# Optimization experiments

Hardware: AMD Instinct MI355X
Metric: run time of the kernel (lower is better)

## Reference

```python
import jax, jax.numpy as jnp
import numpy as np

N, IN_DIM, LDIM = 8192, 512, 256
NEG_SLOPE = 0.01  # torch F.leaky_relu default
EPS = 1e-10


def setup_inputs() -> dict:
    key = jax.random.key(0)
    k1, k2, k3, k4 = jax.random.split(key, 4)
    x = jax.random.normal(k1, (N, IN_DIM), dtype=jnp.float32)
    adj = jax.random.uniform(k2, (N, N), dtype=jnp.float32)
    # nn.Linear(in_dim, learning_dim, bias=False) weight: [learning_dim, in_dim]
    proj_w = jax.random.normal(k3, (LDIM, IN_DIM), dtype=jnp.float32) * (1.0 / np.sqrt(IN_DIM))
    # nn.init.uniform_(learn_w, a=0, b=1)
    learn_w = jax.random.uniform(k4, (LDIM,), dtype=jnp.float32)
    return {"x": x, "adj": adj, "proj_w": proj_w, "learn_w": learn_w}


def reference(x, adj, proj_w, learn_w):
    # x_hat = projection(x): [N, LDIM]
    x_hat = x @ proj_w.T
    # cosine-distance score: sum_d w_d * (1 - xn_i[d] * xn_j[d])
    #   = sum(w) - (xn * w) @ xn.T  -- avoids the N x N x D intermediate
    xn = x_hat / jnp.linalg.norm(x_hat, axis=-1, keepdims=True)  # [N, LDIM]
    scores = jnp.sum(learn_w) - jnp.einsum('id,jd->ij', xn * learn_w, xn)  # [N, N]
    out = jax.nn.leaky_relu(scores, NEG_SLOPE)
    out = out - jnp.max(out, axis=-1, keepdims=True)
    soft_adj = adj * jnp.exp(out)
    soft_adj = soft_adj / jnp.sum(soft_adj, axis=-1, keepdims=True) + EPS
    return soft_adj
```

## Files before the change

### kernel.cpp

```cpp
#include <hip/hip_runtime.h>
#include <stdint.h>

#define NN 8192
#define KDIM 512
#define LDIM 256

typedef short bf16x8 __attribute__((ext_vector_type(8)));
typedef short short8 __attribute__((ext_vector_type(8)));
typedef float f32x4 __attribute__((ext_vector_type(4)));
typedef unsigned short u16x4 __attribute__((ext_vector_type(4)));

__device__ __forceinline__ unsigned short f2bf(float f) {
  unsigned int u = __float_as_uint(f);
  u = (u + 0x7fffu + ((u >> 16) & 1u)) >> 16;
  return (unsigned short)u;
}
__device__ __forceinline__ float bf2f(unsigned short s) {
  return __uint_as_float(((unsigned int)s) << 16);
}

__device__ __forceinline__ void async_ld16(const unsigned short* g, void* l) {
  __builtin_amdgcn_global_load_lds(
      (const __attribute__((address_space(1))) unsigned int*)g,
      (__attribute__((address_space(3))) unsigned int*)l, 16, 0, 0);
}

__global__ __launch_bounds__(256) void cast_kernel(
    const float* __restrict__ x, const float* __restrict__ pw,
    unsigned short* __restrict__ xb, unsigned short* __restrict__ pwb) {
  const int i = blockIdx.x * 256 + threadIdx.x;
  float4 v = ((const float4*)x)[i];
  u16x4 o;
  o[0] = (short)f2bf(v.x); o[1] = (short)f2bf(v.y);
  o[2] = (short)f2bf(v.z); o[3] = (short)f2bf(v.w);
  ((u16x4*)xb)[i] = o;
  if (i < (LDIM * KDIM) / 4) {
    float4 w = ((const float4*)pw)[i];
    u16x4 ow;
    ow[0] = (short)f2bf(w.x); ow[1] = (short)f2bf(w.y);
    ow[2] = (short)f2bf(w.z); ow[3] = (short)f2bf(w.w);
    ((u16x4*)pwb)[i] = ow;
  }
}

__global__ __launch_bounds__(256) void gemm1_norm_kernel(
    const unsigned short* __restrict__ xb,
    const unsigned short* __restrict__ pwb,
    const float* __restrict__ w,
    unsigned short* __restrict__ Ab, unsigned short* __restrict__ Bb) {
  __shared__ alignas(16) unsigned short As[32 * 32];
  __shared__ alignas(16) unsigned short Bs[256 * 32];
  __shared__ float nrm[32][5];
  __shared__ float wS[LDIM];
  __shared__ alignas(16) unsigned short xnS[32][264];
  __shared__ alignas(16) unsigned short anS[32][264];

  const int tid = threadIdx.x;
  const int wave = tid >> 6;
  const int lane = tid & 63;
  const int quad = lane >> 4;
  const int l16 = lane & 15;
  const size_t row0 = (size_t)blockIdx.x * 32;

  if (tid < LDIM) wS[tid] = w[tid];

  f32x4 acc[2][4];
#pragma unroll
  for (int i = 0; i < 2; ++i)
#pragma unroll
    for (int j = 0; j < 4; ++j) acc[i][j] = (f32x4)(0.0f);

  for (int k0 = 0; k0 < KDIM; k0 += 32) {
#pragma unroll
    for (int j = 0; j < 4; ++j) {
      const int c = (wave * 4 + j) * 64 + lane;
      async_ld16(pwb + (size_t)(c >> 2) * KDIM + (c & 3) * 8 + k0,
                 (char*)Bs + (wave * 4 + j) * 1024);
    }
    if (wave == 0) {
#pragma unroll
      for (int j2 = 0; j2 < 2; ++j2) {
        const int c = j2 * 64 + lane;
        async_ld16(xb + (row0 + (c >> 2)) * (size_t)KDIM + (c & 3) * 8 + k0,
                   (char*)As + j2 * 1024);
      }
    }
    __syncthreads();
    bf16x8 av[2], bv[4];
#pragma unroll
    for (int mt = 0; mt < 2; ++mt)
      av[mt] = *(const bf16x8*)(As + (mt * 16 + l16) * 32 + quad * 8);
#pragma unroll
    for (int nt = 0; nt < 4; ++nt)
      bv[nt] = *(const bf16x8*)(Bs + (wave * 64 + nt * 16 + l16) * 32 + quad * 8);
#pragma unroll
    for (int mt = 0; mt < 2; ++mt)
#pragma unroll
      for (int nt = 0; nt < 4; ++nt)
        acc[mt][nt] = __builtin_amdgcn_mfma_f32_16x16x32_bf16(
            av[mt], bv[nt], acc[mt][nt], 0, 0, 0);
    __syncthreads();
  }

#pragma unroll
  for (int mt = 0; mt < 2; ++mt)
#pragma unroll
    for (int r = 0; r < 4; ++r) {
      float s = 0.0f;
#pragma unroll
      for (int nt = 0; nt < 4; ++nt) s += acc[mt][nt][r] * acc[mt][nt][r];
      s += __shfl_xor(s, 1);
      s += __shfl_xor(s, 2);
      s += __shfl_xor(s, 4);
      s += __shfl_xor(s, 8);
      if (l16 == 0) nrm[mt * 16 + quad * 4 + r][wave] = s;
    }
  __syncthreads();
  if (tid < 32)
    nrm[tid][4] = rsqrtf(nrm[tid][0] + nrm[tid][1] + nrm[tid][2] + nrm[tid][3]);
  __syncthreads();

#pragma unroll
  for (int mt = 0; mt < 2; ++mt)
#pragma unroll
    for (int r = 0; r < 4; ++r) {
      const int row = mt * 16 + quad * 4 + r;
      const float inv = nrm[row][4];
#pragma unroll
      for (int nt = 0; nt < 4; ++nt) {
        const int col = wave * 64 + nt * 16 + l16;
        const float xn = acc[mt][nt][r] * inv;
        xnS[row][col] = f2bf(xn);
        anS[row][col] = f2bf(xn * wS[col]);
      }
    }
  __syncthreads();

  {
    const int row = tid >> 3;
    const int cb = (tid & 7) * 32;
    unsigned short* bdst = Bb + (row0 + row) * LDIM + cb;
    unsigned short* adst = Ab + (row0 + row) * LDIM + cb;
#pragma unroll
    for (int q = 0; q < 4; ++q) {
      ((short8*)bdst)[q] = *(const short8*)&xnS[row][cb + q * 8];
      ((short8*)adst)[q] = *(const short8*)&anS[row][cb + q * 8];
    }
  }
}

template <int K, int MODE>
__global__ __launch_bounds__(256) void gemm_bt(
    const unsigned short* __restrict__ A,
    const unsigned short* __restrict__ B,
    float* __restrict__ C,
    unsigned short* __restrict__ T,
    const float* __restrict__ adj,
    float* __restrict__ rowsum) {
  __shared__ unsigned short As[128 * 32];
  __shared__ unsigned short Bs[128 * 32];
  __shared__ float rs[128];
  __shared__ float trans[32 * 132];

  const int tid = threadIdx.x;
  const int wave = tid >> 6;
  const int lane = tid & 63;
  const int quad = lane >> 4;
  const int l16 = lane & 15;
  const int wm = wave >> 1;
  const int wn = wave & 1;

  const int lin = blockIdx.y * 64 + blockIdx.x;
  const int swz = (lin & 7) * 512 + (lin >> 3);
  const size_t row0 = (size_t)(swz >> 6) * 128;
  const size_t col0 = (size_t)(swz & 63) * 128;

  const int c0 = wave * 128 + lane;
  const int mA = c0 >> 2;
  const int kA = (c0 & 3) * 8;
  const unsigned short* Ag = A + (row0 + mA) * (size_t)K + kA;
  const unsigned short* Bg = B + (col0 + mA) * (size_t)K + kA;
  char* AsB = (char*)As;
  char* BsB = (char*)Bs;
  unsigned short* dA0 = (unsigned short*)(AsB + wave * 2048);
  unsigned short* dA1 = (unsigned short*)(AsB + wave * 2048 + 1024);
  unsigned short* dB0 = (unsigned short*)(BsB + wave * 2048);
  unsigned short* dB1 = (unsigned short*)(BsB + wave * 2048 + 1024);

  f32x4 acc[4][4];
#pragma unroll
  for (int i = 0; i < 4; ++i)
#pragma unroll
    for (int j = 0; j < 4; ++j) acc[i][j] = (f32x4)(0.0f);

  for (int k0 = 0; k0 < K; k0 += 32) {
    async_ld16(Ag + k0, dA0);
    async_ld16(Ag + 16 * (size_t)K + k0, dA1);
    async_ld16(Bg + k0, dB0);
    async_ld16(Bg + 16 * (size_t)K + k0, dB1);
    __syncthreads();

    bf16x8 av[4], bv[4];
#pragma unroll
    for (int mt = 0; mt < 4; ++mt)
      av[mt] = *(const bf16x8*)(AsB + (wm * 64 + mt * 16 + l16) * 64 + quad * 16);
#pragma unroll
    for (int nt = 0; nt < 4; ++nt)
      bv[nt] = *(const bf16x8*)(BsB + (wn * 64 + nt * 16 + l16) * 64 + quad * 16);
#pragma unroll
    for (int mt = 0; mt < 4; ++mt)
#pragma unroll
      for (int nt = 0; nt < 4; ++nt)
        acc[mt][nt] = __builtin_amdgcn_mfma_f32_16x16x32_bf16(av[mt], bv[nt], acc[mt][nt], 0, 0, 0);
    __syncthreads();
  }

  const int s = tid >> 3;
  const int cb = tid & 7;
  const int coff = cb * 16;
#pragma unroll
  for (int mt = 0; mt < 4; ++mt) {
    __syncthreads();
#pragma unroll
    for (int nt = 0; nt < 4; ++nt)
#pragma unroll
      for (int r = 0; r < 4; ++r)
        trans[(wm * 16 + quad * 4 + r) * 132 + wn * 64 + nt * 16 + l16] =
            acc[mt][nt][r];
    __syncthreads();
    const size_t gr = row0 + (size_t)(s >> 4) * 64 + mt * 16 + (s & 15);
    const float* arow = adj + gr * NN + col0 + coff;
    float av16[16];
#pragma unroll
    for (int q = 0; q < 4; ++q) {
      float4 a4 = ((const float4*)arow)[q];
      av16[q * 4 + 0] = a4.x;
      av16[q * 4 + 1] = a4.y;
      av16[q * 4 + 2] = a4.z;
      av16[q * 4 + 3] = a4.w;
    }
    const float* drow = &trans[s * 132 + coff];
    float part = 0.0f;
    if constexpr (MODE == 1) {
      short8 p0, p1;
#pragma unroll
      for (int j = 0; j < 16; ++j) {
        float tv = av16[j] * __expf(-drow[j]);
        unsigned short us = f2bf(tv);
        part += bf2f(us);
        if (j < 8) p0[j] = (short)us; else p1[j - 8] = (short)us;
      }
      short8* trow = (short8*)(T + gr * NN + col0 + coff);
      trow[0] = p0;
      trow[1] = p1;
    } else {
      float4 o[4];
#pragma unroll
      for (int j = 0; j < 16; ++j) {
        float tv = av16[j] * __expf(-drow[j]);
        part += tv;
        ((float*)o)[j] = tv;
      }
      float4* crow = (float4*)(C + gr * NN + col0 + coff);
#pragma unroll
      for (int q = 0; q < 4; ++q) crow[q] = o[q];
    }
    part += __shfl_xor(part, 1);
    part += __shfl_xor(part, 2);
    part += __shfl_xor(part, 4);
    if (cb == 0) rs[(s >> 4) * 64 + mt * 16 + (s & 15)] = part;
  }
  __syncthreads();
  if (tid < 128) atomicAdd(&rowsum[row0 + tid], rs[tid]);
}

__global__ __launch_bounds__(256) void scale_bf16_kernel(
    const unsigned short* __restrict__ T, const float* __restrict__ rowsum,
    float* __restrict__ out) {
  const size_t i = (size_t)blockIdx.x * 256 + threadIdx.x;
  const int row = (int)(i >> 10);
  short8 tv = ((const short8*)T)[i];
  const float inv = 1.0f / rowsum[row];
  float4 o0, o1;
  o0.x = bf2f((unsigned short)tv[0]) * inv + 1e-10f;
  o0.y = bf2f((unsigned short)tv[1]) * inv + 1e-10f;
  o0.z = bf2f((unsigned short)tv[2]) * inv + 1e-10f;
  o0.w = bf2f((unsigned short)tv[3]) * inv + 1e-10f;
  o1.x = bf2f((unsigned short)tv[4]) * inv + 1e-10f;
  o1.y = bf2f((unsigned short)tv[5]) * inv + 1e-10f;
  o1.z = bf2f((unsigned short)tv[6]) * inv + 1e-10f;
  o1.w = bf2f((unsigned short)tv[7]) * inv + 1e-10f;
  ((float4*)out)[i * 2] = o0;
  ((float4*)out)[i * 2 + 1] = o1;
}

__global__ __launch_bounds__(256) void scale_f32_kernel(
    float* __restrict__ t, const float* __restrict__ rowsum) {
  const size_t i = (size_t)blockIdx.x * 256 + threadIdx.x;
  const int row = (int)(i >> 11);
  float4 v = ((float4*)t)[i];
  const float inv = 1.0f / rowsum[row];
  v.x = v.x * inv + 1e-10f;
  v.y = v.y * inv + 1e-10f;
  v.z = v.z * inv + 1e-10f;
  v.w = v.w * inv + 1e-10f;
  ((float4*)t)[i] = v;
}

extern "C" void kernel_launch(void* const* d_in, const int* in_sizes, int n_in,
                              void* d_out, int out_size, void* d_ws, size_t ws_size,
                              hipStream_t stream) {
  (void)in_sizes; (void)n_in; (void)out_size;
  const float* x   = (const float*)d_in[0];
  const float* adj = (const float*)d_in[1];
  const float* pw  = (const float*)d_in[2];
  const float* lw  = (const float*)d_in[3];
  float* out = (float*)d_out;
  char* ws = (char*)d_ws;

  unsigned short* xb   = (unsigned short*)(ws);
  unsigned short* pwb  = (unsigned short*)(ws + 8388608);
  unsigned short* Ab   = (unsigned short*)(ws + 17039360);
  unsigned short* Bb   = (unsigned short*)(ws + 21233664);
  float*          rsum = (float*)(ws + 25427968);
  unsigned short* Tbuf = (unsigned short*)(ws + 25460736);
  const bool big_ws = ws_size >= 25460736ull + (size_t)NN * NN * 2ull;

  cast_kernel<<<(NN * KDIM) / (256 * 4), 256, 0, stream>>>(x, pw, xb, pwb);
  gemm1_norm_kernel<<<NN / 32, 256, 0, stream>>>(xb, pwb, lw, Ab, Bb);
  hipMemsetAsync(rsum, 0, NN * sizeof(float), stream);
  if (big_ws) {
    gemm_bt<LDIM, 1><<<dim3(64, 64), 256, 0, stream>>>(Ab, Bb, nullptr, Tbuf, adj, rsum);
    scale_bf16_kernel<<<(NN / 8) * (NN / 256), 256, 0, stream>>>(Tbuf, rsum, out);
  } else {
    gemm_bt<LDIM, 2><<<dim3(64, 64), 256, 0, stream>>>(Ab, Bb, out, nullptr, adj, rsum);
    scale_f32_kernel<<<(NN / 4) * (NN / 256), 256, 0, stream>>>(out, rsum);
  }
}
```

Baseline: 545.5 us.

## Fuse x bf16 cast into projection GEMM and shrink epilogue staging for occupancy

The x-to-bf16 cast moves into the projection GEMM kernel, which loads its 32-row fp32 tile directly into LDS, removing a separate pass that wrote and reread an 8 MB intermediate. The main fused GEMM/softmax kernel halves its epilogue transpose buffer by staging one 64-row half at a time, and adds a launch-bounds occupancy hint of 5 blocks. The cost is more barriers in the epilogue, narrower per-thread adj loads, and a larger LDS footprint in the first GEMM kernel.

```diff
diff --git a/kernel.cpp b/kernel.cpp
--- a/kernel.cpp
+++ b/kernel.cpp
@@ -25,30 +25,22 @@
       (__attribute__((address_space(3))) unsigned int*)l, 16, 0, 0);
 }
 
-__global__ __launch_bounds__(256) void cast_kernel(
-    const float* __restrict__ x, const float* __restrict__ pw,
-    unsigned short* __restrict__ xb, unsigned short* __restrict__ pwb) {
+__global__ __launch_bounds__(256) void cast_pw_kernel(
+    const float* __restrict__ pw, unsigned short* __restrict__ pwb) {
   const int i = blockIdx.x * 256 + threadIdx.x;
-  float4 v = ((const float4*)x)[i];
-  u16x4 o;
-  o[0] = (short)f2bf(v.x); o[1] = (short)f2bf(v.y);
-  o[2] = (short)f2bf(v.z); o[3] = (short)f2bf(v.w);
-  ((u16x4*)xb)[i] = o;
-  if (i < (LDIM * KDIM) / 4) {
-    float4 w = ((const float4*)pw)[i];
-    u16x4 ow;
-    ow[0] = (short)f2bf(w.x); ow[1] = (short)f2bf(w.y);
-    ow[2] = (short)f2bf(w.z); ow[3] = (short)f2bf(w.w);
-    ((u16x4*)pwb)[i] = ow;
-  }
+  float4 w = ((const float4*)pw)[i];
+  u16x4 ow;
+  ow[0] = (short)f2bf(w.x); ow[1] = (short)f2bf(w.y);
+  ow[2] = (short)f2bf(w.z); ow[3] = (short)f2bf(w.w);
+  ((u16x4*)pwb)[i] = ow;
 }
 
 __global__ __launch_bounds__(256) void gemm1_norm_kernel(
-    const unsigned short* __restrict__ xb,
+    const float* __restrict__ x,
     const unsigned short* __restrict__ pwb,
     const float* __restrict__ w,
     unsigned short* __restrict__ Ab, unsigned short* __restrict__ Bb) {
-  __shared__ alignas(16) unsigned short As[32 * 32];
+  __shared__ alignas(16) unsigned short Axl[32 * 520];
   __shared__ alignas(16) unsigned short Bs[256 * 32];
   __shared__ float nrm[32][5];
   __shared__ float wS[LDIM];
@@ -64,6 +56,21 @@
 
   if (tid < LDIM) wS[tid] = w[tid];
 
+  {
+    const float4* xr = (const float4*)(x + row0 * KDIM);
+#pragma unroll
+    for (int rnd = 0; rnd < 16; ++rnd) {
+      const int idx = rnd * 256 + tid;
+      float4 v = xr[idx];
+      u16x4 o;
+      o[0] = (short)f2bf(v.x); o[1] = (short)f2bf(v.y);
+      o[2] = (short)f2bf(v.z); o[3] = (short)f2bf(v.w);
+      const int e = idx * 4;
+      *(u16x4*)&Axl[(e >> 9) * 520 + (e & 511)] = o;
+    }
+  }
+  __syncthreads();
+
   f32x4 acc[2][4];
 #pragma unroll
   for (int i = 0; i < 2; ++i)
@@ -77,19 +84,11 @@
       async_ld16(pwb + (size_t)(c >> 2) * KDIM + (c & 3) * 8 + k0,
                  (char*)Bs + (wave * 4 + j) * 1024);
     }
-    if (wave == 0) {
-#pragma unroll
-      for (int j2 = 0; j2 < 2; ++j2) {
-        const int c = j2 * 64 + lane;
-        async_ld16(xb + (row0 + (c >> 2)) * (size_t)KDIM + (c & 3) * 8 + k0,
-                   (char*)As + j2 * 1024);
-      }
-    }
     __syncthreads();
     bf16x8 av[2], bv[4];
 #pragma unroll
     for (int mt = 0; mt < 2; ++mt)
-      av[mt] = *(const bf16x8*)(As + (mt * 16 + l16) * 32 + quad * 8);
+      av[mt] = *(const bf16x8*)(Axl + (mt * 16 + l16) * 520 + k0 + quad * 8);
 #pragma unroll
     for (int nt = 0; nt < 4; ++nt)
       bv[nt] = *(const bf16x8*)(Bs + (wave * 64 + nt * 16 + l16) * 32 + quad * 8);
@@ -150,7 +149,7 @@
 }
 
 template <int K, int MODE>
-__global__ __launch_bounds__(256) void gemm_bt(
+__global__ __launch_bounds__(256, 5) void gemm_bt(
     const unsigned short* __restrict__ A,
     const unsigned short* __restrict__ B,
     float* __restrict__ C,
@@ -160,7 +159,7 @@
   __shared__ unsigned short As[128 * 32];
   __shared__ unsigned short Bs[128 * 32];
   __shared__ float rs[128];
-  __shared__ float trans[32 * 132];
+  __shared__ float trans[16 * 132];
 
   const int tid = threadIdx.x;
   const int wave = tid >> 6;
@@ -215,60 +214,64 @@
     __syncthreads();
   }
 
-  const int s = tid >> 3;
-  const int cb = tid & 7;
-  const int coff = cb * 16;
+  const int sr = tid >> 4;
+  const int cb = tid & 15;
+  const int coff = cb * 8;
 #pragma unroll
   for (int mt = 0; mt < 4; ++mt) {
-    __syncthreads();
-#pragma unroll
-    for (int nt = 0; nt < 4; ++nt)
-#pragma unroll
-      for (int r = 0; r < 4; ++r)
-        trans[(wm * 16 + quad * 4 + r) * 132 + wn * 64 + nt * 16 + l16] =
-            acc[mt][nt][r];
-    __syncthreads();
-    const size_t gr = row0 + (size_t)(s >> 4) * 64 + mt * 16 + (s & 15);
-    const float* arow = adj + gr * NN + col0 + coff;
-    float av16[16];
-#pragma unroll
-    for (int q = 0; q < 4; ++q) {
-      float4 a4 = ((const float4*)arow)[q];
-      av16[q * 4 + 0] = a4.x;
-      av16[q * 4 + 1] = a4.y;
-      av16[q * 4 + 2] = a4.z;
-      av16[q * 4 + 3] = a4.w;
-    }
-    const float* drow = &trans[s * 132 + coff];
-    float part = 0.0f;
-    if constexpr (MODE == 1) {
-      short8 p0, p1;
-#pragma unroll
-      for (int j = 0; j < 16; ++j) {
-        float tv = av16[j] * __expf(-drow[j]);
-        unsigned short us = f2bf(tv);
-        part += bf2f(us);
-        if (j < 8) p0[j] = (short)us; else p1[j - 8] = (short)us;
+#pragma unroll
+    for (int wh = 0; wh < 2; ++wh) {
+      __syncthreads();
+      if (wm == wh) {
+#pragma unroll
+        for (int nt = 0; nt < 4; ++nt)
+#pragma unroll
+          for (int r = 0; r < 4; ++r)
+            trans[(quad * 4 + r) * 132 + wn * 64 + nt * 16 + l16] =
+                acc[mt][nt][r];
       }
-      short8* trow = (short8*)(T + gr * NN + col0 + coff);
-      trow[0] = p0;
-      trow[1] = p1;
-    } else {
-      float4 o[4];
-#pragma unroll
-      for (int j = 0; j < 16; ++j) {
-        float tv = av16[j] * __expf(-drow[j]);
-        part += tv;
-        ((float*)o)[j] = tv;
+      __syncthreads();
+      const size_t gr = row0 + (size_t)wh * 64 + mt * 16 + sr;
+      const float* arow = adj + gr * NN + col0 + coff;
+      float av8[8];
+#pragma unroll
+      for (int q = 0; q < 2; ++q) {
+        float4 a4 = ((const float4*)arow)[q];
+        av8[q * 4 + 0] = a4.x;
+        av8[q * 4 + 1] = a4.y;
+        av8[q * 4 + 2] = a4.z;
+        av8[q * 4 + 3] = a4.w;
       }
-      float4* crow = (float4*)(C + gr * NN + col0 + coff);
-#pragma unroll
-      for (int q = 0; q < 4; ++q) crow[q] = o[q];
-    }
-    part += __shfl_xor(part, 1);
-    part += __shfl_xor(part, 2);
-    part += __shfl_xor(part, 4);
-    if (cb == 0) rs[(s >> 4) * 64 + mt * 16 + (s & 15)] = part;
+      const float* drow = &trans[sr * 132 + coff];
+      float part = 0.0f;
+      if constexpr (MODE == 1) {
+        short8 p0;
+#pragma unroll
+        for (int j = 0; j < 8; ++j) {
+          float tv = av8[j] * __expf(-drow[j]);
+          unsigned short us = f2bf(tv);
+          part += bf2f(us);
+          p0[j] = (short)us;
+        }
+        *(short8*)(T + gr * NN + col0 + coff) = p0;
+      } else {
+        float4 o[2];
+#pragma unroll
+        for (int j = 0; j < 8; ++j) {
+          float tv = av8[j] * __expf(-drow[j]);
+          part += tv;
+          ((float*)o)[j] = tv;
+        }
+        float4* crow = (float4*)(C + gr * NN + col0 + coff);
+        crow[0] = o[0];
+        crow[1] = o[1];
+      }
+      part += __shfl_xor(part, 1);
+      part += __shfl_xor(part, 2);
+      part += __shfl_xor(part, 4);
+      part += __shfl_xor(part, 8);
+      if (cb == 0) rs[wh * 64 + mt * 16 + sr] = part;
+    }
   }
   __syncthreads();
   if (tid < 128) atomicAdd(&rowsum[row0 + tid], rs[tid]);
@@ -318,7 +321,6 @@
   float* out = (float*)d_out;
   char* ws = (char*)d_ws;
 
-  unsigned short* xb   = (unsigned short*)(ws);
   unsigned short* pwb  = (unsigned short*)(ws + 8388608);
   unsigned short* Ab   = (unsigned short*)(ws + 17039360);
   unsigned short* Bb   = (unsigned short*)(ws + 21233664);
@@ -326,8 +328,8 @@
   unsigned short* Tbuf = (unsigned short*)(ws + 25460736);
   const bool big_ws = ws_size >= 25460736ull + (size_t)NN * NN * 2ull;
 
-  cast_kernel<<<(NN * KDIM) / (256 * 4), 256, 0, stream>>>(x, pw, xb, pwb);
-  gemm1_norm_kernel<<<NN / 32, 256, 0, stream>>>(xb, pwb, lw, Ab, Bb);
+  cast_pw_kernel<<<(LDIM * KDIM) / (256 * 4), 256, 0, stream>>>(pw, pwb);
+  gemm1_norm_kernel<<<NN / 32, 256, 0, stream>>>(x, pwb, lw, Ab, Bb);
   hipMemsetAsync(rsum, 0, NN * sizeof(float), stream);
   if (big_ws) {
     gemm_bt<LDIM, 1><<<dim3(64, 64), 256, 0, stream>>>(Ab, Bb, nullptr, Tbuf, adj, rsum);
```

After: 554.5 us. No clear change (+1.6%).
